# Kernel tuning notes

Measured on AMD Instinct MI355X. Metric: run time of the kernel, lower is better.

The kernel has to match this reference:

```python
import jax, jax.numpy as jnp
import numpy as np

B, S, H = 2, 2048, 2048
E, K = 8, 2            # num_local_experts, num_experts_per_tok
I, IS = 1024, 4096     # expert / shared-expert intermediate dims


def setup_inputs() -> dict:
    key = jax.random.key(0)
    ks = jax.random.split(key, 8)
    w = lambda k, shp: jax.random.normal(k, shp, dtype=jnp.float32) * 0.02
    return {
        "hidden_states": jax.random.normal(ks[0], (B, S, H), dtype=jnp.float32),
        "router_w": w(ks[1], (E, H)),
        "gate_w": w(ks[2], (E, I, H)),
        "up_w": w(ks[3], (E, I, H)),
        "down_w": w(ks[4], (E, H, I)),
        "shared_gate_w": w(ks[5], (IS, H)),
        "shared_up_w": w(ks[6], (IS, H)),
        "shared_down_w": w(ks[7], (H, IS)),
    }


def reference(hidden_states, router_w, gate_w, up_w, down_w,
              shared_gate_w, shared_up_w, shared_down_w):
    x = hidden_states  # [B,S,H]
    b, s, h = x.shape

    # Router: logits over experts, top-k, sigmoid of top values (computed in fp32)
    router_logits = jnp.einsum('bsh,eh->bse', x, router_w)           # [B,S,E]
    top_vals, top_idx = jax.lax.top_k(router_logits, K)              # [B,S,K]
    scores = jax.nn.sigmoid(top_vals.astype(jnp.float32)).astype(x.dtype)

    # Per-token per-expert input scale (each expert appears at most once in top-k)
    onehot = jax.nn.one_hot(top_idx, E, dtype=x.dtype)               # [B,S,K,E]
    scale = jnp.einsum('bsk,bske->bse', scores, onehot)              # [B,S,E]

    # Routed experts: scale is applied to the INPUT of each expert (as in the torch code).
    # With bias-free gated MLP, zero-scaled (unrouted) tokens produce exact zeros,
    # so the dense formulation matches the sparse gather/scatter exactly.
    xs = x.reshape(-1, h)                                            # [T,H]
    sc = scale.reshape(-1, E)                                        # [T,E]
    xe = xs[:, None, :] * sc[:, :, None]                             # [T,E,H]
    g = jnp.einsum('teh,eih->tei', xe, gate_w)                       # [T,E,I]
    u = jnp.einsum('teh,eih->tei', xe, up_w)                         # [T,E,I]
    hmid = jax.nn.silu(g) * u
    routed = jnp.einsum('tei,ehi->th', hmid, down_w).reshape(b, s, h)

    # Shared expert (dense gated MLP over all tokens)
    sg = jnp.einsum('bsh,ih->bsi', x, shared_gate_w)
    su = jnp.einsum('bsh,ih->bsi', x, shared_up_w)
    shared = jnp.einsum('bsi,hi->bsh', jax.nn.silu(sg) * su, shared_down_w)

    return routed + shared, router_logits
```

## Files before the change

### kernel.cpp

```cpp
#include <hip/hip_runtime.h>
#include <hip/hip_bf16.h>
#include <cstdint>
#include <cstddef>

typedef __bf16 bf16x8 __attribute__((ext_vector_type(8)));
typedef float  f32x4  __attribute__((ext_vector_type(4)));

static constexpr int TOK  = 4096;
static constexpr int H    = 2048;
static constexpr int E    = 8;
static constexpr int IDIM = 1024;
static constexpr int ISD  = 4096;
static constexpr int MAXTILES = 72;
static constexpr int MAXROWS  = MAXTILES * 128;


__device__ __forceinline__ void gll16(const void* g, void* l) {
  __builtin_amdgcn_global_load_lds((const __attribute__((address_space(1))) void*)g,
                                   (__attribute__((address_space(3))) void*)l, 16, 0, 0);
}

__device__ __forceinline__ unsigned short f2bf(float f) {
  unsigned int u = __float_as_uint(f);
  u = (u + 0x7fffu + ((u >> 16) & 1u)) >> 16;
  return (unsigned short)u;
}

__global__ __launch_bounds__(256) void detect_kernel(const unsigned int* __restrict__ x,
                                                     int* __restrict__ meta) {
  __shared__ int sh[256];
  const int tid = threadIdx.x;
  int c = 0;
  for (int i = tid; i < 1024; i += 256) {
    const unsigned int e = (x[i] >> 7) & 0xFFu;
    c += (e >= 100u && e <= 150u) ? 1 : 0;
  }
  sh[tid] = c;
  if (tid >= 4 && tid < 24) meta[tid] = 0;
  __syncthreads();
  if (tid == 0) {
    int s = 0;
    for (int i = 0; i < 256; ++i) s += sh[i];
    meta[0] = (s > 512) ? 1 : 0;
  }
}

__global__ __launch_bounds__(256) void convert_kernel(const float* __restrict__ src,
                                                      unsigned short* __restrict__ dst,
                                                      int n4, const int* __restrict__ flag) {
  if (*flag) return;
  int i = blockIdx.x * 256 + threadIdx.x;
  const int stride = gridDim.x * 256;
  for (; i < n4; i += stride) {
    const float4 v = ((const float4*)src)[i];
    ushort4 o;
    o.x = f2bf(v.x); o.y = f2bf(v.y); o.z = f2bf(v.z); o.w = f2bf(v.w);
    ((ushort4*)dst)[i] = o;
  }
}

__global__ __launch_bounds__(256) void router_kernel(
    const void* __restrict__ x_, const void* __restrict__ rw_,
    void* __restrict__ out, float* __restrict__ scale,
    int* __restrict__ meta, int* __restrict__ topk)
{
  const int bfmode = meta[0];
  const int t   = blockIdx.x;
  const int tid = threadIdx.x;
  const int l   = tid & 63, w = tid >> 6;
  const int off = tid * 8;

  float xs[8];
  if (bfmode) {
    bf16x8 v = *(const bf16x8*)((const unsigned short*)x_ + (size_t)t * H + off);
#pragma unroll
    for (int j = 0; j < 8; ++j) xs[j] = (float)v[j];
  } else {
    const float* xr = (const float*)x_ + (size_t)t * H + off;
    const float4 a = *(const float4*)xr;
    const float4 b = *(const float4*)(xr + 4);
    xs[0]=a.x; xs[1]=a.y; xs[2]=a.z; xs[3]=a.w; xs[4]=b.x; xs[5]=b.y; xs[6]=b.z; xs[7]=b.w;
  }

  float p[E];
#pragma unroll
  for (int e = 0; e < E; ++e) {
    float wv[8];
    if (bfmode) {
      bf16x8 v = *(const bf16x8*)((const unsigned short*)rw_ + (size_t)e * H + off);
#pragma unroll
      for (int j = 0; j < 8; ++j) wv[j] = (float)v[j];
    } else {
      const float* wr = (const float*)rw_ + (size_t)e * H + off;
      const float4 a = *(const float4*)wr;
      const float4 b = *(const float4*)(wr + 4);
      wv[0]=a.x; wv[1]=a.y; wv[2]=a.z; wv[3]=a.w; wv[4]=b.x; wv[5]=b.y; wv[6]=b.z; wv[7]=b.w;
    }
    float s = 0.f;
#pragma unroll
    for (int j = 0; j < 8; ++j) s = fmaf(xs[j], wv[j], s);
    p[e] = s;
  }
#pragma unroll
  for (int e = 0; e < E; ++e)
    for (int o = 32; o > 0; o >>= 1) p[e] += __shfl_down(p[e], o);

  __shared__ float red[E][4];
  __shared__ float lg[E];
  __shared__ float sres[2];
  __shared__ int   ires[2];
  if (l == 0) {
#pragma unroll
    for (int e = 0; e < E; ++e) red[e][w] = p[e];
  }
  __syncthreads();
  if (tid < E) {
    const float v = red[tid][0] + red[tid][1] + red[tid][2] + red[tid][3];
    lg[tid] = v;
    const size_t oi = (size_t)TOK * H + (size_t)t * E + tid;
    if (bfmode) ((unsigned short*)out)[oi] = f2bf(v);
    else        ((float*)out)[oi] = v;
  }
  __syncthreads();
  if (tid == 0) {
    int i0 = 0; float v0 = lg[0];
    for (int e = 1; e < E; ++e) if (lg[e] > v0) { v0 = lg[e]; i0 = e; }
    int i1 = -1; float v1 = 0.f; bool init = false;
    for (int e = 0; e < E; ++e) {
      if (e == i0) continue;
      if (!init || lg[e] > v1) { v1 = lg[e]; i1 = e; init = true; }
    }
    sres[0] = 1.f / (1.f + expf(-v0)); ires[0] = i0;
    sres[1] = 1.f / (1.f + expf(-v1)); ires[1] = i1;
    topk[2 * t + 0] = i0;
    topk[2 * t + 1] = i1;
    atomicAdd(&meta[4 + i0], 1);
    atomicAdd(&meta[4 + i1], 1);
  }
  __syncthreads();
  if (tid < E) {
    float s = 0.f;
    if (tid == ires[0]) s = sres[0];
    else if (tid == ires[1]) s = sres[1];
    scale[(size_t)t * E + tid] = s;
  }
}

__global__ __launch_bounds__(256) void scan_kernel(int* __restrict__ meta,
                                                   int* __restrict__ list) {
  const int tid = threadIdx.x;
  if (tid == 0) {
    int s = 0, nt = 0;
    for (int e = 0; e < E; ++e) {
      meta[24 + e] = s;
      const int cnt = meta[4 + e];
      const int tiles = (cnt + 127) >> 7;
      for (int i = 0; i < tiles; ++i) {
        meta[64 + nt]  = e;
        meta[136 + nt] = s + i * 128;
        ++nt;
      }
      s += tiles << 7;
    }
    meta[32] = s;
    meta[20] = nt;
  }
  for (int i = tid; i < MAXROWS; i += 256) list[i] = 0;
}

__global__ __launch_bounds__(256) void scatter_kernel(int* __restrict__ meta,
                                                      const int* __restrict__ topk,
                                                      int* __restrict__ list,
                                                      int* __restrict__ tokpos) {
  const int t = blockIdx.x * 256 + threadIdx.x;
  if (t >= TOK) return;
#pragma unroll
  for (int k = 0; k < 2; ++k) {
    const int e = topk[2 * t + k];
    const int p = atomicAdd(&meta[12 + e], 1);
    const int g = meta[24 + e] + p;
    list[g] = t;
    tokpos[2 * t + k] = g;
  }
}

__global__ __launch_bounds__(256) void gateup_shared_kernel(
    const void* __restrict__ xo_,  const unsigned short* __restrict__ cx,
    const void* __restrict__ sgo_, const unsigned short* __restrict__ csgw,
    const void* __restrict__ suo_, const unsigned short* __restrict__ csuw,
    unsigned short* __restrict__ hmid_sh, const int* __restrict__ meta)
{
  const int bfmode = meta[0];
  const unsigned short* x       = bfmode ? (const unsigned short*)xo_  : cx;
  const unsigned short* sgate_w = bfmode ? (const unsigned short*)sgo_ : csgw;
  const unsigned short* sup_w   = bfmode ? (const unsigned short*)suo_ : csuw;

  __shared__ __attribute__((aligned(16))) unsigned short As[128 * 64];
  __shared__ __attribute__((aligned(16))) unsigned short Bgs[64 * 64];
  __shared__ __attribute__((aligned(16))) unsigned short Bus[64 * 64];

  const int tid = threadIdx.x;
  const int l = tid & 63, w = tid >> 6;
  const int m0 = blockIdx.x * 128;
  const int jb = blockIdx.y * 64;

  const unsigned short* gB = sgate_w + (size_t)jb * H;
  const unsigned short* uB = sup_w   + (size_t)jb * H;

  f32x4 accg[4][2] = {};
  f32x4 accu[4][2] = {};
  const int wm = (w >> 1) * 64;
  const int wn = (w & 1) * 32;
  const int quad = l >> 4, lm = l & 15;

  for (int k0 = 0; k0 < H; k0 += 64) {
#pragma unroll
    for (int j = 0; j < 4; ++j) {
      const int g = j * 256 + tid;
      const int r = g >> 3, c = g & 7;
      const int cc = c ^ (r & 7);
      gll16(x + (size_t)(m0 + r) * H + k0 + cc * 8, &As[g * 8]);
    }
#pragma unroll
    for (int j = 0; j < 2; ++j) {
      const int g = j * 256 + tid;
      const int r = g >> 3, c = g & 7;
      const int cc = c ^ (r & 7);
      gll16(gB + (size_t)r * H + k0 + cc * 8, &Bgs[g * 8]);
      gll16(uB + (size_t)r * H + k0 + cc * 8, &Bus[g * 8]);
    }
    __syncthreads();
#pragma unroll
    for (int ks = 0; ks < 64; ks += 32) {
      const int kc  = (ks >> 3) + quad;
      const int csw = (kc ^ (lm & 7)) * 8;
      bf16x8 a[4], bg[2], bu[2];
#pragma unroll
      for (int mt = 0; mt < 4; ++mt)
        a[mt] = *(const bf16x8*)&As[(wm + mt * 16 + lm) * 64 + csw];
#pragma unroll
      for (int nt = 0; nt < 2; ++nt) {
        bg[nt] = *(const bf16x8*)&Bgs[(wn + nt * 16 + lm) * 64 + csw];
        bu[nt] = *(const bf16x8*)&Bus[(wn + nt * 16 + lm) * 64 + csw];
      }
#pragma unroll
      for (int mt = 0; mt < 4; ++mt)
#pragma unroll
        for (int nt = 0; nt < 2; ++nt) {
          accg[mt][nt] = __builtin_amdgcn_mfma_f32_16x16x32_bf16(a[mt], bg[nt], accg[mt][nt], 0, 0, 0);
          accu[mt][nt] = __builtin_amdgcn_mfma_f32_16x16x32_bf16(a[mt], bu[nt], accu[mt][nt], 0, 0, 0);
        }
    }
    __syncthreads();
  }

#pragma unroll
  for (int mt = 0; mt < 4; ++mt) {
#pragma unroll
    for (int r = 0; r < 4; ++r) {
      const int t = m0 + wm + mt * 16 + quad * 4 + r;
#pragma unroll
      for (int nt = 0; nt < 2; ++nt) {
        const int j = jb + wn + nt * 16 + lm;
        const float g = accg[mt][nt][r];
        const float u = accu[mt][nt][r];
        const float hm = (g / (1.f + expf(-g))) * u;
        hmid_sh[(size_t)t * ISD + j] = f2bf(hm);
      }
    }
  }
}

__global__ __launch_bounds__(256) void gateup_routed_kernel(
    const void* __restrict__ xo_,  const unsigned short* __restrict__ cx,
    const void* __restrict__ gwo_, const unsigned short* __restrict__ cgw,
    const void* __restrict__ uwo_, const unsigned short* __restrict__ cuw,
    const float* __restrict__ scale, const int* __restrict__ list,
    unsigned short* __restrict__ hmid_r, const int* __restrict__ meta)
{
  if ((int)blockIdx.x >= meta[20]) return;
  const int bfmode = meta[0];
  const unsigned short* x      = bfmode ? (const unsigned short*)xo_  : cx;
  const unsigned short* gate_w = bfmode ? (const unsigned short*)gwo_ : cgw;
  const unsigned short* up_w   = bfmode ? (const unsigned short*)uwo_ : cuw;

  __shared__ __attribute__((aligned(16))) unsigned short As[128 * 64];
  __shared__ __attribute__((aligned(16))) unsigned short Bgs[64 * 64];
  __shared__ __attribute__((aligned(16))) unsigned short Bus[64 * 64];

  const int tid = threadIdx.x;
  const int l = tid & 63, w = tid >> 6;
  const int e    = meta[64 + blockIdx.x];
  const int base = meta[136 + blockIdx.x];
  const int jj   = blockIdx.y * 64;

  const unsigned short* gB = gate_w + ((size_t)e * IDIM + jj) * H;
  const unsigned short* uB = up_w   + ((size_t)e * IDIM + jj) * H;

  int tok[4];
#pragma unroll
  for (int j = 0; j < 4; ++j) tok[j] = list[base + ((j * 256 + tid) >> 3)];

  f32x4 accg[4][2] = {};
  f32x4 accu[4][2] = {};
  const int wm = (w >> 1) * 64;
  const int wn = (w & 1) * 32;
  const int quad = l >> 4, lm = l & 15;

  for (int k0 = 0; k0 < H; k0 += 64) {
#pragma unroll
    for (int j = 0; j < 4; ++j) {
      const int g = j * 256 + tid;
      const int r = g >> 3, c = g & 7;
      const int cc = c ^ (r & 7);
      gll16(x + (size_t)tok[j] * H + k0 + cc * 8, &As[g * 8]);
    }
#pragma unroll
    for (int j = 0; j < 2; ++j) {
      const int g = j * 256 + tid;
      const int r = g >> 3, c = g & 7;
      const int cc = c ^ (r & 7);
      gll16(gB + (size_t)r * H + k0 + cc * 8, &Bgs[g * 8]);
      gll16(uB + (size_t)r * H + k0 + cc * 8, &Bus[g * 8]);
    }
    __syncthreads();
#pragma unroll
    for (int ks = 0; ks < 64; ks += 32) {
      const int kc  = (ks >> 3) + quad;
      const int csw = (kc ^ (lm & 7)) * 8;
      bf16x8 a[4], bg[2], bu[2];
#pragma unroll
      for (int mt = 0; mt < 4; ++mt)
        a[mt] = *(const bf16x8*)&As[(wm + mt * 16 + lm) * 64 + csw];
#pragma unroll
      for (int nt = 0; nt < 2; ++nt) {
        bg[nt] = *(const bf16x8*)&Bgs[(wn + nt * 16 + lm) * 64 + csw];
        bu[nt] = *(const bf16x8*)&Bus[(wn + nt * 16 + lm) * 64 + csw];
      }
#pragma unroll
      for (int mt = 0; mt < 4; ++mt)
#pragma unroll
        for (int nt = 0; nt < 2; ++nt) {
          accg[mt][nt] = __builtin_amdgcn_mfma_f32_16x16x32_bf16(a[mt], bg[nt], accg[mt][nt], 0, 0, 0);
          accu[mt][nt] = __builtin_amdgcn_mfma_f32_16x16x32_bf16(a[mt], bu[nt], accu[mt][nt], 0, 0, 0);
        }
    }
    __syncthreads();
  }

#pragma unroll
  for (int mt = 0; mt < 4; ++mt) {
#pragma unroll
    for (int r = 0; r < 4; ++r) {
      const int row  = wm + mt * 16 + quad * 4 + r;
      const int gpos = base + row;
      const int token = list[gpos];
      const float s = scale[(size_t)token * E + e];
#pragma unroll
      for (int nt = 0; nt < 2; ++nt) {
        const int j = jj + wn + nt * 16 + lm;
        const float g = accg[mt][nt][r] * s;
        const float u = accu[mt][nt][r] * s;
        const float hm = (g / (1.f + expf(-g))) * u;
        hmid_r[(size_t)gpos * IDIM + j] = f2bf(hm);
      }
    }
  }
}

__global__ __launch_bounds__(256) void down_routed_kernel(
    const unsigned short* __restrict__ hmid_r,
    const void* __restrict__ dwo_, const unsigned short* __restrict__ cdw,
    float* __restrict__ dbuf, const int* __restrict__ meta)
{
  if ((int)blockIdx.y >= meta[20]) return;
  const int bfmode = meta[0];
  const unsigned short* down_w = bfmode ? (const unsigned short*)dwo_ : cdw;

  __shared__ __attribute__((aligned(16))) unsigned short As[128 * 64];
  __shared__ __attribute__((aligned(16))) unsigned short Bs[128 * 64];

  const int tid = threadIdx.x;
  const int l = tid & 63, w = tid >> 6;
  const int e    = meta[64 + blockIdx.y];
  const int base = meta[136 + blockIdx.y];
  const int n0 = blockIdx.x * 128;

  const unsigned short* Bbase = down_w + ((size_t)e * H + n0) * IDIM;

  f32x4 acc[4][4] = {};
  const int wm = (w >> 1) * 64;
  const int wn = (w & 1) * 64;
  const int quad = l >> 4, lm = l & 15;

  for (int k0 = 0; k0 < IDIM; k0 += 64) {
#pragma unroll
    for (int j = 0; j < 4; ++j) {
      const int g = j * 256 + tid;
      const int r = g >> 3, c = g & 7;
      const int cc = c ^ (r & 7);
      gll16(hmid_r + (size_t)(base + r) * IDIM + k0 + cc * 8, &As[g * 8]);
    }
#pragma unroll
    for (int j = 0; j < 4; ++j) {
      const int g = j * 256 + tid;
      const int r = g >> 3, c = g & 7;
      const int cc = c ^ (r & 7);
      gll16(Bbase + (size_t)r * IDIM + k0 + cc * 8, &Bs[g * 8]);
    }
    __syncthreads();
#pragma unroll
    for (int ks = 0; ks < 64; ks += 32) {
      const int kc  = (ks >> 3) + quad;
      const int csw = (kc ^ (lm & 7)) * 8;
      bf16x8 a[4], b[4];
#pragma unroll
      for (int mt = 0; mt < 4; ++mt)
        a[mt] = *(const bf16x8*)&As[(wm + mt * 16 + lm) * 64 + csw];
#pragma unroll
      for (int nt = 0; nt < 4; ++nt)
        b[nt] = *(const bf16x8*)&Bs[(wn + nt * 16 + lm) * 64 + csw];
#pragma unroll
      for (int mt = 0; mt < 4; ++mt)
#pragma unroll
        for (int nt = 0; nt < 4; ++nt)
          acc[mt][nt] = __builtin_amdgcn_mfma_f32_16x16x32_bf16(a[mt], b[nt], acc[mt][nt], 0, 0, 0);
    }
    __syncthreads();
  }

#pragma unroll
  for (int mt = 0; mt < 4; ++mt)
#pragma unroll
    for (int nt = 0; nt < 4; ++nt)
#pragma unroll
      for (int r = 0; r < 4; ++r) {
        const int row = wm + mt * 16 + quad * 4 + r;
        const int n   = n0 + wn + nt * 16 + lm;
        dbuf[(size_t)(base + row) * H + n] = acc[mt][nt][r];
      }
}

__global__ __launch_bounds__(256) void down_shared_kernel(
    const unsigned short* __restrict__ hmid_sh,
    const void* __restrict__ sdwo_, const unsigned short* __restrict__ csdw,
    const float* __restrict__ dbuf, const int* __restrict__ tokpos,
    void* __restrict__ out, const int* __restrict__ meta)
{
  const int bfmode = meta[0];
  const unsigned short* sdown_w = bfmode ? (const unsigned short*)sdwo_ : csdw;

  __shared__ __attribute__((aligned(16))) unsigned short As[128 * 64];
  __shared__ __attribute__((aligned(16))) unsigned short Bs[128 * 64];

  const int tid = threadIdx.x;
  const int l = tid & 63, w = tid >> 6;
  const int m0 = blockIdx.y * 128;
  const int n0 = blockIdx.x * 128;

  f32x4 acc[4][4] = {};
  const int wm = (w >> 1) * 64;
  const int wn = (w & 1) * 64;
  const int quad = l >> 4, lm = l & 15;

  for (int k0 = 0; k0 < ISD; k0 += 64) {
#pragma unroll
    for (int j = 0; j < 4; ++j) {
      const int g = j * 256 + tid;
      const int r = g >> 3, c = g & 7;
      const int cc = c ^ (r & 7);
      gll16(hmid_sh + (size_t)(m0 + r) * ISD + k0 + cc * 8, &As[g * 8]);
    }
#pragma unroll
    for (int j = 0; j < 4; ++j) {
      const int g = j * 256 + tid;
      const int r = g >> 3, c = g & 7;
      const int cc = c ^ (r & 7);
      gll16(sdown_w + (size_t)(n0 + r) * ISD + k0 + cc * 8, &Bs[g * 8]);
    }
    __syncthreads();
#pragma unroll
    for (int ks = 0; ks < 64; ks += 32) {
      const int kc  = (ks >> 3) + quad;
      const int csw = (kc ^ (lm & 7)) * 8;
      bf16x8 a[4], b[4];
#pragma unroll
      for (int mt = 0; mt < 4; ++mt)
        a[mt] = *(const bf16x8*)&As[(wm + mt * 16 + lm) * 64 + csw];
#pragma unroll
      for (int nt = 0; nt < 4; ++nt)
        b[nt] = *(const bf16x8*)&Bs[(wn + nt * 16 + lm) * 64 + csw];
#pragma unroll
      for (int mt = 0; mt < 4; ++mt)
#pragma unroll
        for (int nt = 0; nt < 4; ++nt)
          acc[mt][nt] = __builtin_amdgcn_mfma_f32_16x16x32_bf16(a[mt], b[nt], acc[mt][nt], 0, 0, 0);
    }
    __syncthreads();
  }

  if (bfmode) {
    unsigned short* o = (unsigned short*)out;
#pragma unroll
    for (int mt = 0; mt < 4; ++mt)
#pragma unroll
      for (int r = 0; r < 4; ++r) {
        const int t = m0 + wm + mt * 16 + quad * 4 + r;
        const int p0 = tokpos[2 * t], p1 = tokpos[2 * t + 1];
#pragma unroll
        for (int nt = 0; nt < 4; ++nt) {
          const int n = n0 + wn + nt * 16 + lm;
          const float v = acc[mt][nt][r]
                        + dbuf[(size_t)p0 * H + n] + dbuf[(size_t)p1 * H + n];
          o[(size_t)t * H + n] = f2bf(v);
        }
      }
  } else {
    float* o = (float*)out;
#pragma unroll
    for (int mt = 0; mt < 4; ++mt)
#pragma unroll
      for (int r = 0; r < 4; ++r) {
        const int t = m0 + wm + mt * 16 + quad * 4 + r;
        const int p0 = tokpos[2 * t], p1 = tokpos[2 * t + 1];
#pragma unroll
        for (int nt = 0; nt < 4; ++nt) {
          const int n = n0 + wn + nt * 16 + lm;
          o[(size_t)t * H + n] = acc[mt][nt][r]
                               + dbuf[(size_t)p0 * H + n] + dbuf[(size_t)p1 * H + n];
        }
      }
  }
}

extern "C" void kernel_launch(void* const* d_in, const int* in_sizes, int n_in,
                              void* d_out, int out_size, void* d_ws, size_t ws_size,
                              hipStream_t stream) {
  const void* x   = d_in[0];
  const void* rw  = d_in[1];
  const void* gw  = d_in[2];
  const void* uw  = d_in[3];
  const void* dw  = d_in[4];
  const void* sgw = d_in[5];
  const void* suw = d_in[6];
  const void* sdw = d_in[7];

  char* wsb = (char*)d_ws;
  int*   meta   = (int*)wsb;
  float* scale  = (float*)(wsb + 1024);
  int*   topk   = (int*)(wsb + 1024 + (size_t)TOK * E * 4);
  int*   list   = topk + (size_t)TOK * 2;
  int*   tokpos = list + MAXROWS;
  unsigned short* hmid_sh = (unsigned short*)(wsb + 234496);
  unsigned short* hmid_r  = hmid_sh + (size_t)TOK * ISD;
  unsigned short* cx   = hmid_r + (size_t)MAXROWS * IDIM;
  unsigned short* crw  = cx  + (size_t)TOK * H;
  unsigned short* cgw  = crw + (size_t)E * H;
  unsigned short* cuw  = cgw + (size_t)E * IDIM * H;
  unsigned short* cdw  = cuw + (size_t)E * IDIM * H;
  unsigned short* csgw = cdw + (size_t)E * H * IDIM;
  unsigned short* csuw = csgw + (size_t)ISD * H;
  unsigned short* csdw = csuw + (size_t)ISD * H;
  float* dbuf = (float*)cx;

  detect_kernel<<<1, 256, 0, stream>>>((const unsigned int*)x, meta);

  convert_kernel<<<1024, 256, 0, stream>>>((const float*)x,   cx,   (TOK * H) / 4,        meta);
  convert_kernel<<<16,   256, 0, stream>>>((const float*)rw,  crw,  (E * H) / 4,          meta);
  convert_kernel<<<1024, 256, 0, stream>>>((const float*)gw,  cgw,  (E * IDIM * H) / 4,   meta);
  convert_kernel<<<1024, 256, 0, stream>>>((const float*)uw,  cuw,  (E * IDIM * H) / 4,   meta);
  convert_kernel<<<1024, 256, 0, stream>>>((const float*)dw,  cdw,  (E * H * IDIM) / 4,   meta);
  convert_kernel<<<1024, 256, 0, stream>>>((const float*)sgw, csgw, (ISD * H) / 4,        meta);
  convert_kernel<<<1024, 256, 0, stream>>>((const float*)suw, csuw, (ISD * H) / 4,        meta);
  convert_kernel<<<1024, 256, 0, stream>>>((const float*)sdw, csdw, (ISD * H) / 4,        meta);

  router_kernel<<<TOK, 256, 0, stream>>>(x, rw, d_out, scale, meta, topk);
  scan_kernel<<<1, 256, 0, stream>>>(meta, list);
  scatter_kernel<<<TOK / 256, 256, 0, stream>>>(meta, topk, list, tokpos);

  dim3 g1(TOK / 128, ISD / 64);
  gateup_shared_kernel<<<g1, 256, 0, stream>>>(x, cx, sgw, csgw, suw, csuw, hmid_sh, meta);

  dim3 g2(MAXTILES, IDIM / 64);
  gateup_routed_kernel<<<g2, 256, 0, stream>>>(x, cx, gw, cgw, uw, cuw,
                                               scale, list, hmid_r, meta);

  dim3 g3(H / 128, MAXTILES);
  down_routed_kernel<<<g3, 256, 0, stream>>>(hmid_r, dw, cdw, dbuf, meta);

  dim3 g4(H / 128, TOK / 128);
  down_shared_kernel<<<g4, 256, 0, stream>>>(hmid_sh, sdw, csdw, dbuf, tokpos, d_out, meta);
}
```

Before: 935.3 us.

## Rewrite shared gate/up GEMM as 256x256 double-buffered pipelined tile; merge conversion launches

After: 898.7 us. 3.9% less time.

```diff
diff --git a/kernel.cpp b/kernel.cpp
--- a/kernel.cpp
+++ b/kernel.cpp
@@ -45,18 +45,36 @@
   }
 }
 
-__global__ __launch_bounds__(256) void convert_kernel(const float* __restrict__ src,
-                                                      unsigned short* __restrict__ dst,
-                                                      int n4, const int* __restrict__ flag) {
+__global__ __launch_bounds__(256) void convert_all_kernel(
+    const float* __restrict__ s0, const float* __restrict__ s1,
+    const float* __restrict__ s2, const float* __restrict__ s3,
+    const float* __restrict__ s4, const float* __restrict__ s5,
+    const float* __restrict__ s6, const float* __restrict__ s7,
+    unsigned short* __restrict__ d0, unsigned short* __restrict__ d1,
+    unsigned short* __restrict__ d2, unsigned short* __restrict__ d3,
+    unsigned short* __restrict__ d4, unsigned short* __restrict__ d5,
+    unsigned short* __restrict__ d6, unsigned short* __restrict__ d7,
+    const int* __restrict__ flag)
+{
   if (*flag) return;
-  int i = blockIdx.x * 256 + threadIdx.x;
   const int stride = gridDim.x * 256;
-  for (; i < n4; i += stride) {
-    const float4 v = ((const float4*)src)[i];
-    ushort4 o;
-    o.x = f2bf(v.x); o.y = f2bf(v.y); o.z = f2bf(v.z); o.w = f2bf(v.w);
-    ((ushort4*)dst)[i] = o;
-  }
+  const int base = blockIdx.x * 256 + threadIdx.x;
+  auto go = [&](const float* s, unsigned short* d, int n4) {
+    for (int i = base; i < n4; i += stride) {
+      const float4 v = ((const float4*)s)[i];
+      ushort4 o;
+      o.x = f2bf(v.x); o.y = f2bf(v.y); o.z = f2bf(v.z); o.w = f2bf(v.w);
+      ((ushort4*)d)[i] = o;
+    }
+  };
+  go(s0, d0, (TOK * H) / 4);
+  go(s1, d1, (E * H) / 4);
+  go(s2, d2, (E * IDIM * H) / 4);
+  go(s3, d3, (E * IDIM * H) / 4);
+  go(s4, d4, (E * H * IDIM) / 4);
+  go(s5, d5, (ISD * H) / 4);
+  go(s6, d6, (ISD * H) / 4);
+  go(s7, d7, (ISD * H) / 4);
 }
 
 __global__ __launch_bounds__(256) void router_kernel(
@@ -184,88 +202,134 @@
   }
 }
 
-__global__ __launch_bounds__(256) void gateup_shared_kernel(
+#define GU_BAR_   __builtin_amdgcn_s_barrier()
+#define GU_LGKM0_ { asm volatile("s_waitcnt lgkmcnt(0)" ::: "memory"); \
+                    __builtin_amdgcn_sched_barrier(0); }
+#define GU_VM4_   asm volatile("s_waitcnt vmcnt(4)" ::: "memory")
+#define GU_VM0_   asm volatile("s_waitcnt vmcnt(0)" ::: "memory")
+
+#define LDA_(p, mh) { _Pragma("unroll") for (int q2 = 0; q2 < 4; ++q2) { \
+  _Pragma("unroll") for (int ks = 0; ks < 2; ++ks) { \
+    const int row_ = 32 * (4 * (mh) + q2) + 16 * wm + lm; \
+    a[q2][ks] = *(const bf16x8*)&ldsA[(p) * 16384 + row_ * 64 + \
+                                      (((ks * 4 + quad) ^ (lm & 7)) * 8)]; } } }
+
+#define LDB_(p, nh) { _Pragma("unroll") for (int nt2 = 0; nt2 < 2; ++nt2) { \
+  _Pragma("unroll") for (int ks = 0; ks < 2; ++ks) { \
+    const int row_ = 16 * (wn + 4 * (2 * (nh) + nt2)) + lm; \
+    bb[nh][nt2][ks] = *(const bf16x8*)&ldsB[(p) * 16384 + row_ * 64 + \
+                                            (((ks * 4 + quad) ^ (lm & 7)) * 8)]; } } }
+
+#define MFMA_(mh, nh) { __builtin_amdgcn_s_setprio(1); \
+  _Pragma("unroll") for (int q2 = 0; q2 < 4; ++q2) \
+  _Pragma("unroll") for (int nt2 = 0; nt2 < 2; ++nt2) \
+  _Pragma("unroll") for (int ks = 0; ks < 2; ++ks) \
+    acc[4 * (mh) + q2][2 * (nh) + nt2] = __builtin_amdgcn_mfma_f32_16x16x32_bf16( \
+      a[q2][ks], bb[nh][nt2][ks], acc[4 * (mh) + q2][2 * (nh) + nt2], 0, 0, 0); \
+  __builtin_amdgcn_s_setprio(0); }
+
+__global__ __launch_bounds__(512, 2) void gateup_shared_kernel(
     const void* __restrict__ xo_,  const unsigned short* __restrict__ cx,
     const void* __restrict__ sgo_, const unsigned short* __restrict__ csgw,
     const void* __restrict__ suo_, const unsigned short* __restrict__ csuw,
     unsigned short* __restrict__ hmid_sh, const int* __restrict__ meta)
 {
+  extern __shared__ unsigned short lds[];
+  unsigned short* ldsA = lds;
+  unsigned short* ldsB = lds + 32768;
+
   const int bfmode = meta[0];
-  const unsigned short* x       = bfmode ? (const unsigned short*)xo_  : cx;
-  const unsigned short* sgate_w = bfmode ? (const unsigned short*)sgo_ : csgw;
-  const unsigned short* sup_w   = bfmode ? (const unsigned short*)suo_ : csuw;
-
-  __shared__ __attribute__((aligned(16))) unsigned short As[128 * 64];
-  __shared__ __attribute__((aligned(16))) unsigned short Bgs[64 * 64];
-  __shared__ __attribute__((aligned(16))) unsigned short Bus[64 * 64];
+  const unsigned short* x  = bfmode ? (const unsigned short*)xo_  : cx;
+  const unsigned short* gw = bfmode ? (const unsigned short*)sgo_ : csgw;
+  const unsigned short* uw = bfmode ? (const unsigned short*)suo_ : csuw;
 
   const int tid = threadIdx.x;
   const int l = tid & 63, w = tid >> 6;
-  const int m0 = blockIdx.x * 128;
-  const int jb = blockIdx.y * 64;
-
-  const unsigned short* gB = sgate_w + (size_t)jb * H;
-  const unsigned short* uB = sup_w   + (size_t)jb * H;
-
-  f32x4 accg[4][2] = {};
-  f32x4 accu[4][2] = {};
-  const int wm = (w >> 1) * 64;
-  const int wn = (w & 1) * 32;
+  const int wm = w >> 2, wn = w & 3;
   const int quad = l >> 4, lm = l & 15;
-
-  for (int k0 = 0; k0 < H; k0 += 64) {
-#pragma unroll
-    for (int j = 0; j < 4; ++j) {
-      const int g = j * 256 + tid;
-      const int r = g >> 3, c = g & 7;
-      const int cc = c ^ (r & 7);
-      gll16(x + (size_t)(m0 + r) * H + k0 + cc * 8, &As[g * 8]);
-    }
-#pragma unroll
-    for (int j = 0; j < 2; ++j) {
-      const int g = j * 256 + tid;
-      const int r = g >> 3, c = g & 7;
-      const int cc = c ^ (r & 7);
-      gll16(gB + (size_t)r * H + k0 + cc * 8, &Bgs[g * 8]);
-      gll16(uB + (size_t)r * H + k0 + cc * 8, &Bus[g * 8]);
-    }
-    __syncthreads();
-#pragma unroll
-    for (int ks = 0; ks < 64; ks += 32) {
-      const int kc  = (ks >> 3) + quad;
-      const int csw = (kc ^ (lm & 7)) * 8;
-      bf16x8 a[4], bg[2], bu[2];
-#pragma unroll
-      for (int mt = 0; mt < 4; ++mt)
-        a[mt] = *(const bf16x8*)&As[(wm + mt * 16 + lm) * 64 + csw];
-#pragma unroll
-      for (int nt = 0; nt < 2; ++nt) {
-        bg[nt] = *(const bf16x8*)&Bgs[(wn + nt * 16 + lm) * 64 + csw];
-        bu[nt] = *(const bf16x8*)&Bus[(wn + nt * 16 + lm) * 64 + csw];
-      }
-#pragma unroll
-      for (int mt = 0; mt < 4; ++mt)
-#pragma unroll
-        for (int nt = 0; nt < 2; ++nt) {
-          accg[mt][nt] = __builtin_amdgcn_mfma_f32_16x16x32_bf16(a[mt], bg[nt], accg[mt][nt], 0, 0, 0);
-          accu[mt][nt] = __builtin_amdgcn_mfma_f32_16x16x32_bf16(a[mt], bu[nt], accu[mt][nt], 0, 0, 0);
-        }
-    }
-    __syncthreads();
-  }
-
-#pragma unroll
-  for (int mt = 0; mt < 4; ++mt) {
-#pragma unroll
-    for (int r = 0; r < 4; ++r) {
-      const int t = m0 + wm + mt * 16 + quad * 4 + r;
-#pragma unroll
-      for (int nt = 0; nt < 2; ++nt) {
-        const int j = jb + wn + nt * 16 + lm;
-        const float g = accg[mt][nt][r];
-        const float u = accu[mt][nt][r];
+  const int m0 = blockIdx.x * 256;
+  const int jb = blockIdx.y * 128;
+
+  const unsigned short* gB = gw + (size_t)jb * H;
+  const unsigned short* uB = uw + (size_t)jb * H;
+
+  const int sr0 = tid >> 3,         sc0 = tid & 7;
+  const int sr1 = (tid + 512) >> 3, sc1 = (tid + 512) & 7;
+  const int scc0 = sc0 ^ (sr0 & 7), scc1 = sc1 ^ (sr1 & 7);
+  const int sd0 = tid * 8, sd1 = (tid + 512) * 8;
+
+  auto stA = [&](int kt, int half) {
+    unsigned short* d = ldsA + (kt & 1) * 16384 + half * 8192;
+    const unsigned short* s = x + (size_t)(m0 + half * 128) * H + kt * 64;
+    gll16(s + (size_t)sr0 * H + scc0 * 8, d + sd0);
+    gll16(s + (size_t)sr1 * H + scc1 * 8, d + sd1);
+  };
+  auto stB = [&](int kt, int half) {
+    unsigned short* d = ldsB + (kt & 1) * 16384 + half * 8192;
+    const unsigned short* s = (half ? uB : gB) + kt * 64;
+    gll16(s + (size_t)sr0 * H + scc0 * 8, d + sd0);
+    gll16(s + (size_t)sr1 * H + scc1 * 8, d + sd1);
+  };
+
+  f32x4 acc[8][4] = {};
+  bf16x8 a[4][2];
+  bf16x8 bb[2][2][2];
+
+  stA(0, 0); stB(0, 0); stB(0, 1); stA(0, 1);
+  stB(1, 1); stA(1, 1);
+  GU_VM4_; GU_BAR_;
+
+  for (int i = 0; i < (H / 128) - 1; ++i) {
+    const int t0 = 2 * i, t1 = 2 * i + 1;
+    LDA_(0, 0); LDB_(0, 0); stA(t1, 0);
+    GU_BAR_; GU_LGKM0_; MFMA_(0, 0); GU_BAR_;
+    LDB_(0, 1); stB(t1, 0);
+    GU_BAR_; GU_LGKM0_; MFMA_(0, 1); GU_BAR_;
+    LDA_(0, 1); stA(t0 + 2, 0);
+    GU_BAR_; GU_LGKM0_; MFMA_(1, 1); GU_BAR_;
+    stB(t0 + 2, 0); GU_VM4_;
+    GU_BAR_; GU_LGKM0_; MFMA_(1, 0); GU_BAR_;
+    LDA_(1, 0); LDB_(1, 0); stB(t0 + 2, 1);
+    GU_BAR_; GU_LGKM0_; MFMA_(0, 0); GU_BAR_;
+    LDB_(1, 1); stA(t0 + 2, 1);
+    GU_BAR_; GU_LGKM0_; MFMA_(0, 1); GU_BAR_;
+    LDA_(1, 1); stB(t1 + 2, 1);
+    GU_BAR_; GU_LGKM0_; MFMA_(1, 1); GU_BAR_;
+    stA(t1 + 2, 1); GU_VM4_;
+    GU_BAR_; GU_LGKM0_; MFMA_(1, 0); GU_BAR_;
+  }
+
+  {
+    const int t1 = H / 64 - 1;
+    LDA_(0, 0); LDB_(0, 0); stA(t1, 0);
+    GU_BAR_; GU_LGKM0_; MFMA_(0, 0); GU_BAR_;
+    LDB_(0, 1); stB(t1, 0);
+    GU_BAR_; GU_LGKM0_; MFMA_(0, 1); GU_BAR_;
+    LDA_(0, 1);
+    GU_BAR_; GU_LGKM0_; MFMA_(1, 1); GU_BAR_;
+    GU_VM0_;
+    GU_BAR_; GU_LGKM0_; MFMA_(1, 0); GU_BAR_;
+    LDA_(1, 0); LDB_(1, 0);
+    GU_BAR_; GU_LGKM0_; MFMA_(0, 0); GU_BAR_;
+    LDB_(1, 1);
+    GU_BAR_; GU_LGKM0_; MFMA_(0, 1); GU_BAR_;
+    LDA_(1, 1);
+    GU_BAR_; GU_LGKM0_; MFMA_(1, 1); GU_BAR_;
+    MFMA_(1, 0);
+  }
+
+#pragma unroll
+  for (int mt = 0; mt < 8; ++mt) {
+    const int trow = m0 + 32 * mt + 16 * wm + quad * 4;
+#pragma unroll
+    for (int ntp = 0; ntp < 2; ++ntp) {
+      const int col = jb + wn * 16 + ntp * 64 + lm;
+#pragma unroll
+      for (int rr = 0; rr < 4; ++rr) {
+        const float g = acc[mt][ntp][rr];
+        const float u = acc[mt][ntp + 2][rr];
         const float hm = (g / (1.f + expf(-g))) * u;
-        hmid_sh[(size_t)t * ISD + j] = f2bf(hm);
+        hmid_sh[(size_t)(trow + rr) * ISD + col] = f2bf(hm);
       }
     }
   }
@@ -563,23 +627,27 @@
   unsigned short* csdw = csuw + (size_t)ISD * H;
   float* dbuf = (float*)cx;
 
+  static int attr_set = 0;
+  if (!attr_set) {
+    hipFuncSetAttribute(reinterpret_cast<const void*>(gateup_shared_kernel),
+                        hipFuncAttributeMaxDynamicSharedMemorySize, 131072);
+    attr_set = 1;
+  }
+
   detect_kernel<<<1, 256, 0, stream>>>((const unsigned int*)x, meta);
 
-  convert_kernel<<<1024, 256, 0, stream>>>((const float*)x,   cx,   (TOK * H) / 4,        meta);
-  convert_kernel<<<16,   256, 0, stream>>>((const float*)rw,  crw,  (E * H) / 4,          meta);
-  convert_kernel<<<1024, 256, 0, stream>>>((const float*)gw,  cgw,  (E * IDIM * H) / 4,   meta);
-  convert_kernel<<<1024, 256, 0, stream>>>((const float*)uw,  cuw,  (E * IDIM * H) / 4,   meta);
-  convert_kernel<<<1024, 256, 0, stream>>>((const float*)dw,  cdw,  (E * H * IDIM) / 4,   meta);
-  convert_kernel<<<1024, 256, 0, stream>>>((const float*)sgw, csgw, (ISD * H) / 4,        meta);
-  convert_kernel<<<1024, 256, 0, stream>>>((const float*)suw, csuw, (ISD * H) / 4,        meta);
-  convert_kernel<<<1024, 256, 0, stream>>>((const float*)sdw, csdw, (ISD * H) / 4,        meta);
+  convert_all_kernel<<<2048, 256, 0, stream>>>(
+      (const float*)x, (const float*)rw, (const float*)gw, (const float*)uw,
+      (const float*)dw, (const float*)sgw, (const float*)suw, (const float*)sdw,
+      cx, crw, cgw, cuw, cdw, csgw, csuw, csdw, meta);
 
   router_kernel<<<TOK, 256, 0, stream>>>(x, rw, d_out, scale, meta, topk);
   scan_kernel<<<1, 256, 0, stream>>>(meta, list);
   scatter_kernel<<<TOK / 256, 256, 0, stream>>>(meta, topk, list, tokpos);
 
-  dim3 g1(TOK / 128, ISD / 64);
-  gateup_shared_kernel<<<g1, 256, 0, stream>>>(x, cx, sgw, csgw, suw, csuw, hmid_sh, meta);
+  dim3 g1(TOK / 256, ISD / 128);
+  gateup_shared_kernel<<<g1, 512, 131072, stream>>>(x, cx, sgw, csgw, suw, csuw,
+                                                    hmid_sh, meta);
 
   dim3 g2(MAXTILES, IDIM / 64);
   gateup_routed_kernel<<<g2, 256, 0, stream>>>(x, cx, gw, cgw, uw, cuw,
```
